# Optimization experiments

Hardware: AMD Instinct MI355X
Metric: run time of the kernel (lower is better)

## Reference

```python
import jax, jax.numpy as jnp
import numpy as np

N_NODES = 25000
N_EDGES = 400000
N_GRAPHS = 100
D_IN = 16
D = 32          # node_dim
K = 11          # spectral coefficients = edge_dim
NOUT1 = 30
NOUT2 = 2
L = 2           # n_interactions
D_OUT = 32


def setup_inputs() -> dict:
    key = jax.random.key(0)
    ks = jax.random.split(key, 24)
    s = 0.1
    inp = {
        'x': jax.random.normal(ks[0], (N_NODES, D_IN), jnp.float32),
        'edge_attr': jax.random.uniform(ks[1], (N_EDGES, K), jnp.float32),
        'edge_index': jax.random.randint(ks[2], (2, N_EDGES), 0, N_NODES),
        'batch': jnp.sort(jax.random.randint(ks[3], (N_NODES,), 0, N_GRAPHS)),
        # embedding
        'emb_w': jax.random.normal(ks[4], (D_IN, D)) * s,
        'emb_b': jnp.zeros((D,)),
        # per-interaction params, stacked on leading L axis
        'init_w': jax.random.normal(ks[5], (L, D, D)) * s,             # initial_dense (no bias)
        'e1_w': jax.random.normal(ks[6], (L, K, 2 * K)) * s,
        'e2_w': jax.random.normal(ks[7], (L, K, 2 * K)) * s,
        'e3_w': jax.random.normal(ks[8], (L, K, 2 * K)) * s,
        'e4_w': jax.random.normal(ks[9], (L, 4 * K, K)) * s,
        'conv_w': jax.random.normal(ks[10], (L, K, D, NOUT1)) * s,     # SpectConv weight (selfconn=False)
        'conv_b': jnp.zeros((L, NOUT1)),
        'att_v': jax.random.normal(ks[11], (L, D, 1)) * s,
        'skip1_w': jax.random.normal(ks[12], (L, D, NOUT2)) * s,
        'skip1_b': jnp.full((L, NOUT2), 0.01),
        'skip2_w': jax.random.normal(ks[13], (L, D, NOUT2)) * s,
        'skip2_b': jnp.full((L, NOUT2), 0.01),
        'out_w': jax.random.normal(ks[14], (L, NOUT1 + NOUT2, D)) * s,
        'out_b': jnp.full((L, D), 0.01),
        # encoder output head
        'final_w': jax.random.normal(ks[15], (D, D_OUT)) * s,
        'final_b': jnp.zeros((D_OUT,)),
    }
    return inp


def _segment_softmax(raw, dst, n):
    m = jax.ops.segment_max(raw, dst, num_segments=n)
    m = jnp.where(jnp.isfinite(m), m, 0.0)
    e = jnp.exp(raw - m[dst])
    denom = jax.ops.segment_sum(e, dst, num_segments=n)
    return e / (denom[dst] + 1e-16)


def _interaction(h, src, dst, edge_attr, p):
    (init_w, e1_w, e2_w, e3_w, e4_w, conv_w, conv_b, att_v,
     s1_w, s1_b, s2_w, s2_b, out_w, out_b) = p
    n = h.shape[0]
    h_proj = h @ init_w                                     # [N, D]
    # learned edge transform
    lin = jax.nn.relu(edge_attr @ e1_w)                     # [E, 2K]
    gate = jnp.tanh(edge_attr @ e2_w) * jnp.tanh(edge_attr @ e3_w)
    ea = jax.nn.relu(jnp.concatenate([lin, gate], axis=1) @ e4_w)  # [E, K]
    # spectral conv with attention (selfconn=False)
    xs = h_proj[src]                                        # gather [E, D]
    msgs = ea[:, :, None] * xs[:, None, :]                  # [E, K, D]
    agg = jax.ops.segment_sum(msgs, dst, num_segments=n)    # [N, K, D]
    sum_out = jnp.einsum('nkd,kdo->no', agg, conv_w)        # [N, NOUT1]
    pooled = ea.mean(axis=1, keepdims=True) * xs            # mean_k msg_k, [E, D]
    raw_att = (pooled @ att_v)[:, 0]                        # [E]
    att = _segment_softmax(raw_att, dst, n)                 # [E]
    att_agg = jax.ops.segment_sum(att[:, None, None] * msgs, dst, num_segments=n)
    att_out = jnp.einsum('nkd,kdo->no', att_agg, conv_w)
    conv_out = jax.nn.relu(sum_out + att_out + conv_b)      # [N, NOUT1]
    skip = jnp.tanh(h_proj @ s1_w + s1_b) * jnp.tanh(h_proj @ s2_w + s2_b)  # [N, NOUT2]
    layer_out = jnp.concatenate([conv_out, skip], axis=1)
    delta = layer_out @ out_w + out_b                       # [N, D]
    return delta, att


def reference(x, edge_attr, emb_w, emb_b, init_w, e1_w, e2_w, e3_w, e4_w,
              conv_w, conv_b, att_v, skip1_w, skip1_b, skip2_w, skip2_b,
              out_w, out_b, final_w, final_b, edge_index, batch):
    src, dst = edge_index[0], edge_index[1]
    h = x @ emb_w + emb_b                                   # node embedding [N, D]
    atts = []
    for l in range(L):
        p = (init_w[l], e1_w[l], e2_w[l], e3_w[l], e4_w[l], conv_w[l], conv_b[l],
             att_v[l], skip1_w[l], skip1_b[l], skip2_w[l], skip2_b[l], out_w[l], out_b[l])
        delta, att = _interaction(h, src, dst, edge_attr, p)
        h = h + delta                                       # residual
        atts.append(att)
    # global mean pool per graph
    counts = jax.ops.segment_sum(jnp.ones((h.shape[0],), h.dtype), batch, num_segments=N_GRAPHS)
    pooled = jax.ops.segment_sum(h, batch, num_segments=N_GRAPHS) / jnp.maximum(counts, 1.0)[:, None]
    output = pooled @ final_w + final_b                     # [G, D_OUT]
    return output, h, jnp.stack(atts)
```

## Files before the change

### kernel.cpp

```cpp
#include <hip/hip_runtime.h>
#include <hip/hip_bf16.h>

typedef __hip_bfloat16 bf16;
using f32x4v = __attribute__((ext_vector_type(4))) float;
using bf16x8 = __attribute__((ext_vector_type(8))) short;

#define N_NODES 25000
#define N_PAD   25024
#define N_EDGES 400000
#define N_GR    100
#define SCAN_C  25

__device__ __forceinline__ bf16 tob(float v) { return __float2bfloat16(v); }
__device__ __forceinline__ unsigned short tobu(float v) {
  union { bf16 b; unsigned short u; } c; c.b = __float2bfloat16(v); return c.u;
}
__device__ __forceinline__ float b2f(unsigned short u) { return __uint_as_float(((unsigned)u) << 16); }
__device__ __forceinline__ float tanh_fast(float x) {
  float e = __expf(2.f * x);
  return 1.f - 2.f * __builtin_amdgcn_rcpf(e + 1.f);
}

__global__ __launch_bounds__(256) void hist_kernel(const int* __restrict__ dst, int* __restrict__ deg, int E) {
  int e = blockIdx.x * blockDim.x + threadIdx.x;
  if (e < E) atomicAdd(&deg[dst[e]], 1);
}

__global__ __launch_bounds__(1024) void scan_kernel(const int* __restrict__ deg, int* __restrict__ offs,
                                                    int* __restrict__ cur, int n) {
  __shared__ int wsum[16];
  __shared__ int wpre[16];
  int t = threadIdx.x, lane = t & 63, w = t >> 6;
  int base = t * SCAN_C;
  int loc[SCAN_C];
  int s = 0;
  #pragma unroll
  for (int i = 0; i < SCAN_C; i++) {
    int idx = base + i;
    int v = (idx < n) ? deg[idx] : 0;
    loc[i] = s; s += v;
  }
  int x = s;
  #pragma unroll
  for (int sh = 1; sh < 64; sh <<= 1) { int y = __shfl_up(x, sh); if (lane >= sh) x += y; }
  if (lane == 63) wsum[w] = x;
  __syncthreads();
  if (w == 0 && lane < 16) {
    int ws_ = wsum[lane], xs = ws_;
    #pragma unroll
    for (int sh = 1; sh < 16; sh <<= 1) { int y = __shfl_up(xs, sh); if (lane >= sh) xs += y; }
    wpre[lane] = xs - ws_;
  }
  __syncthreads();
  int excl = wpre[w] + x - s;
  #pragma unroll
  for (int i = 0; i < SCAN_C; i++) {
    int idx = base + i;
    if (idx < n) { int o = excl + loc[i]; offs[idx] = o; cur[idx] = o; }
  }
  if (t == 1023) offs[n] = excl + s;
}

__global__ __launch_bounds__(256) void prep_kernel(const float* __restrict__ e1, const float* __restrict__ e2,
                                                   const float* __restrict__ e3, const float* __restrict__ e4,
                                                   const float* __restrict__ attv, const float* __restrict__ convw,
                                                   const float* __restrict__ outw,
                                                   const int* __restrict__ batch,
                                                   float* __restrict__ wE, bf16* __restrict__ Wt,
                                                   bf16* __restrict__ owB, int* __restrict__ gb,
                                                   int* __restrict__ deg) {
  int i = blockIdx.x * blockDim.x + threadIdx.x;
  if (i < N_NODES) deg[i] = 0;
  if (i < 2 * 1352) {
    int l = i / 1352, r = i % 1352;
    float v = 0.f;
    if (r < 264)       { int q = r;        int j = q / 12, k = q % 12; if (k < 11) v = e1[l*242 + k*22 + j]; }
    else if (r < 528)  { int q = r - 264;  int j = q / 12, k = q % 12; if (k < 11) v = e2[l*242 + k*22 + j]; }
    else if (r < 792)  { int q = r - 528;  int j = q / 12, k = q % 12; if (k < 11) v = e3[l*242 + k*22 + j]; }
    else if (r < 1056) { int q = r - 792;  int j = q / 12, k = q % 12; if (k < 11) v = e4[l*484 + j*11 + k]; }
    else if (r < 1320) { int q = r - 1056; int j = q / 12, k = q % 12; if (k < 11) v = e4[l*484 + (22 + j)*11 + k]; }
    else               { int d = r - 1320; v = attv[l*32 + d]; }
    wE[i] = v;
  }
  int t = i - 2 * 1352;
  if (t >= 0 && t < 2 * 32 * 352) {
    int l = t / (32 * 352), q = t % (32 * 352);
    int o = q / 352, dk = q % 352;
    int d = dk / 11, kk = dk % 11;
    float v = 0.f;
    if (o < 30) v = convw[l*10560 + (kk*32 + d)*30 + o];
    Wt[t] = tob(v);
  }
  int u = i - 2 * 1352 - 2 * 32 * 352;
  if (u >= 0 && u < 2048) {
    int l = u >> 10, rem = u & 1023;
    int hf = rem >> 9, rem2 = rem & 511;
    int lane = rem2 >> 3, j = rem2 & 7;
    int k = (lane >> 4) * 8 + j, n = lane & 15;
    owB[u] = tob(outw[l*1024 + k*32 + hf*16 + n]);
  }
  int g = i - 2 * 1352 - 2 * 32 * 352 - 2048;
  if (g >= 0 && g <= N_GR) {
    if (g == N_GR) { gb[g] = N_NODES; }
    else {
      int lo = 0, hi = N_NODES;
      while (lo < hi) { int mid = (lo + hi) >> 1; if (batch[mid] < g) lo = mid + 1; else hi = mid; }
      gb[g] = lo;
    }
  }
}

__global__ __launch_bounds__(256) void emb_hproj_kernel(const float* __restrict__ x, const float* __restrict__ w,
                                                        const float* __restrict__ b, const float* __restrict__ w1,
                                                        float* __restrict__ h, float* __restrict__ hp,
                                                        unsigned short* __restrict__ hpb, int N) {
  __shared__ float semb[16 * 32];
  __shared__ float sw1[32 * 32];
  __shared__ float sb[32];
  __shared__ float sx[8][16];
  __shared__ float sh[8][33];
  int tid = threadIdx.x;
  for (int i = tid; i < 16 * 32; i += 256) semb[i] = w[i];
  for (int i = tid; i < 32 * 32; i += 256) sw1[i] = w1[i];
  if (tid < 32) sb[tid] = b[tid];
  int nb = blockIdx.x * 8;
  if (tid < 128) {
    int n = nb + (tid >> 4), k = tid & 15;
    sx[tid >> 4][k] = (n < N) ? x[(size_t)n * 16 + k] : 0.f;
  }
  __syncthreads();
  int grp = tid >> 5, d = tid & 31;
  int n = nb + grp;
  float acc = sb[d];
  #pragma unroll
  for (int k = 0; k < 16; k++) acc += sx[grp][k] * semb[k*32 + d];
  sh[grp][d] = acc;
  if (n < N) h[(size_t)n * 32 + d] = acc;
  __syncthreads();
  float hpv = 0.f;
  #pragma unroll
  for (int k = 0; k < 32; k++) hpv += sh[grp][k] * sw1[k*32 + d];
  if (n < N) {
    hp[(size_t)n * 32 + d] = hpv;
    hpb[(size_t)n * 32 + d] = tobu(hpv);
  }
}

__device__ __forceinline__ void loadw12(const float4* base, int idx3, float* w) {
  float4 a = base[idx3], b = base[idx3 + 1], c = base[idx3 + 2];
  w[0]=a.x; w[1]=a.y; w[2]=a.z; w[3]=a.w;
  w[4]=b.x; w[5]=b.y; w[6]=b.z; w[7]=b.w;
  w[8]=c.x; w[9]=c.y; w[10]=c.z; w[11]=c.w;
}

__global__ __launch_bounds__(256) void edge_kernel(const float* __restrict__ eattr,
                                                   const int* __restrict__ srcA,
                                                   const int* __restrict__ dstA,
                                                   int* __restrict__ cur,
                                                   int* __restrict__ elist,
                                                   int* __restrict__ epos,
                                                   const unsigned short* __restrict__ hpb,
                                                   const float* __restrict__ wEl,
                                                   uint4* __restrict__ pay, int first, int E) {
  const float4* w4 = (const float4*)wEl;
  int e = blockIdx.x * blockDim.x + threadIdx.x;
  bool live = e < E;
  float a[11], acc[11];
  #pragma unroll
  for (int k = 0; k < 11; k++) {
    a[k] = live ? eattr[(size_t)e*11 + k] : 0.f;
    acc[k] = 0.f;
  }
  int pp = 0;
  if (live) {
    if (first) {
      pp = atomicAdd(&cur[dstA[e]], 1);
      elist[pp] = e;
      epos[e] = pp;
    } else {
      pp = epos[e];
    }
  }
  for (int j = 0; j < 22; j++) {
    float w[12];
    loadw12(w4, j*3, w);
    float l1 = 0.f;
    #pragma unroll
    for (int k = 0; k < 11; k++) l1 += a[k] * w[k];
    loadw12(w4, 66 + j*3, w);
    float l2 = 0.f;
    #pragma unroll
    for (int k = 0; k < 11; k++) l2 += a[k] * w[k];
    loadw12(w4, 132 + j*3, w);
    float l3 = 0.f;
    #pragma unroll
    for (int k = 0; k < 11; k++) l3 += a[k] * w[k];
    float gg = tanh_fast(l2) * tanh_fast(l3);
    l1 = fmaxf(l1, 0.f);
    float wl[12], wg[12];
    loadw12(w4, 198 + j*3, wl);
    loadw12(w4, 264 + j*3, wg);
    #pragma unroll
    for (int k = 0; k < 11; k++) acc[k] += l1*wl[k] + gg*wg[k];
  }
  if (!live) return;
  const float* av = wEl + 1320;
  float mean = 0.f;
  #pragma unroll
  for (int k = 0; k < 11; k++) { acc[k] = fmaxf(acc[k], 0.f); mean += acc[k]; }
  mean *= (1.f / 11.f);
  int s = srcA[e];
  const uint2* hb = (const uint2*)(hpb + (size_t)s * 32);
  float dot = 0.f;
  #pragma unroll
  for (int q = 0; q < 8; q++) {
    uint2 hv = hb[q];
    dot += b2f((unsigned short)hv.x) * av[q*4+0] + b2f((unsigned short)(hv.x >> 16)) * av[q*4+1]
         + b2f((unsigned short)hv.y) * av[q*4+2] + b2f((unsigned short)(hv.y >> 16)) * av[q*4+3];
  }
  float raw = mean * dot;
  unsigned p[6];
  #pragma unroll
  for (int q = 0; q < 5; q++)
    p[q] = (unsigned)tobu(acc[2*q]) | ((unsigned)tobu(acc[2*q+1]) << 16);
  p[5] = (unsigned)tobu(acc[10]);
  pay[(size_t)pp * 2]     = make_uint4(p[0], p[1], p[2], p[3]);
  pay[(size_t)pp * 2 + 1] = make_uint4(p[4], p[5], __float_as_uint(raw), (unsigned)s);
}

__device__ __forceinline__ void unpack_pay(uint4 p0, uint4 p1, float* ev) {
  ev[0] = b2f((unsigned short)p0.x); ev[1] = b2f((unsigned short)(p0.x >> 16));
  ev[2] = b2f((unsigned short)p0.y); ev[3] = b2f((unsigned short)(p0.y >> 16));
  ev[4] = b2f((unsigned short)p0.z); ev[5] = b2f((unsigned short)(p0.z >> 16));
  ev[6] = b2f((unsigned short)p0.w); ev[7] = b2f((unsigned short)(p0.w >> 16));
  ev[8] = b2f((unsigned short)p1.x); ev[9] = b2f((unsigned short)(p1.x >> 16));
  ev[10] = b2f((unsigned short)p1.y);
}

__global__ __launch_bounds__(256) void node_kernel(const int* __restrict__ offs, const int* __restrict__ elist,
                                                   const uint4* __restrict__ pay,
                                                   const unsigned short* __restrict__ hpb,
                                                   bf16* __restrict__ Abuf, float* __restrict__ atts, int N) {
  int wid = threadIdx.x >> 6, lane = threadIdx.x & 63;
  int half = lane >> 5, d = lane & 31;
  int n = blockIdx.x * 4 + wid;
  if (n >= N_PAD) return;
  int beg = 0, deg = 0;
  if (n < N) { beg = offs[n]; deg = offs[n + 1] - beg; }
  const float* payf = (const float*)pay;

  float M, inv;
  float einv_reg = 0.f;
  bool fast = (deg <= 64);
  if (fast) {
    float r = (lane < deg) ? payf[(size_t)(beg + lane) * 8 + 6] : -1e30f;
    float mm = r;
    #pragma unroll
    for (int sh = 1; sh < 64; sh <<= 1) mm = fmaxf(mm, __shfl_xor(mm, sh));
    M = mm;
    float ex = (lane < deg) ? __expf(r - M) : 0.f;
    float ss = ex;
    #pragma unroll
    for (int sh = 1; sh < 64; sh <<= 1) ss += __shfl_xor(ss, sh);
    inv = 1.f / (ss + 1e-16f);
    einv_reg = ex * inv;
    if (lane < deg) atts[elist[beg + lane]] = einv_reg;
  } else {
    float m_l = -1e30f;
    for (int jj = lane; jj < deg; jj += 64)
      m_l = fmaxf(m_l, payf[(size_t)(beg + jj) * 8 + 6]);
    #pragma unroll
    for (int sh = 1; sh < 64; sh <<= 1) m_l = fmaxf(m_l, __shfl_xor(m_l, sh));
    M = m_l;
    float s_l = 0.f;
    for (int jj = lane; jj < deg; jj += 64)
      s_l += __expf(payf[(size_t)(beg + jj) * 8 + 6] - M);
    #pragma unroll
    for (int sh = 1; sh < 64; sh <<= 1) s_l += __shfl_xor(s_l, sh);
    inv = 1.f / (s_l + 1e-16f);
    for (int jj = lane; jj < deg; jj += 64) {
      float r = payf[(size_t)(beg + jj) * 8 + 6];
      atts[elist[beg + jj]] = __expf(r - M) * inv;
    }
  }

  float agg[11];
  #pragma unroll
  for (int k = 0; k < 11; k++) agg[k] = 0.f;

  int j = half;
  for (; j + 2 < deg; j += 4) {
    uint4 a0 = pay[(size_t)(beg + j) * 2],     a1 = pay[(size_t)(beg + j) * 2 + 1];
    uint4 b0 = pay[(size_t)(beg + j + 2) * 2], b1 = pay[(size_t)(beg + j + 2) * 2 + 1];
    float xa = b2f(hpb[(size_t)(int)a1.w * 32 + d]);
    float xb = b2f(hpb[(size_t)(int)b1.w * 32 + d]);
    float ca = fast ? (1.f + __shfl(einv_reg, j))
                    : (1.f + __expf(__uint_as_float(a1.z) - M) * inv);
    float cb = fast ? (1.f + __shfl(einv_reg, j + 2))
                    : (1.f + __expf(__uint_as_float(b1.z) - M) * inv);
    float cxa = ca * xa, cxb = cb * xb;
    float eva[11], evb[11];
    unpack_pay(a0, a1, eva);
    unpack_pay(b0, b1, evb);
    #pragma unroll
    for (int k = 0; k < 11; k++) agg[k] += eva[k] * cxa + evb[k] * cxb;
  }
  for (; j < deg; j += 2) {
    uint4 q0 = pay[(size_t)(beg + j) * 2], q1 = pay[(size_t)(beg + j) * 2 + 1];
    float xs = b2f(hpb[(size_t)(int)q1.w * 32 + d]);
    float c = fast ? (1.f + __shfl(einv_reg, j))
                   : (1.f + __expf(__uint_as_float(q1.z) - M) * inv);
    float cx = c * xs;
    float ev[11];
    unpack_pay(q0, q1, ev);
    #pragma unroll
    for (int k = 0; k < 11; k++) agg[k] += ev[k] * cx;
  }

  #pragma unroll
  for (int k = 0; k < 11; k++) agg[k] += __shfl_xor(agg[k], 32);

  if (half == 0) {
    bf16* arow = Abuf + (size_t)n * 352 + d * 11;
    #pragma unroll
    for (int k = 0; k < 11; k++) arow[k] = tob(agg[k]);
  }
}

__global__ __launch_bounds__(128) void convfused_kernel(const short* __restrict__ A, const short* __restrict__ Wt,
                                                        const short* __restrict__ owB,
                                                        const float* __restrict__ hp, float* __restrict__ h,
                                                        const float* __restrict__ convb,
                                                        const float* __restrict__ s1w, const float* __restrict__ s1b,
                                                        const float* __restrict__ s2w, const float* __restrict__ s2b,
                                                        const float* __restrict__ outb,
                                                        const float* __restrict__ initw_next,
                                                        float* __restrict__ hp_out, unsigned short* __restrict__ hpb_out,
                                                        int N) {
  __shared__ short slo[32][40];
  __shared__ float sdelta[32][36];
  __shared__ float sskipw[128];
  __shared__ float sskipb[4];
  __shared__ float scb[32];
  __shared__ float sob[32];
  __shared__ float sw1[1024];
  int tid = threadIdx.x;
  if (tid < 64) sskipw[tid] = s1w[tid];
  if (tid >= 64 && tid < 128) sskipw[tid] = s2w[tid - 64];
  if (tid < 32) sob[tid] = outb[tid];
  if (tid >= 32 && tid < 64) scb[tid - 32] = (tid - 32 < 30) ? convb[tid - 32] : 0.f;
  if (tid >= 96 && tid < 100) sskipb[tid - 96] = (tid < 98) ? s1b[tid - 96] : s2b[tid - 98];
  if (initw_next) {
    for (int i = tid; i < 1024; i += 128) sw1[i] = initw_next[i];
  }
  __syncthreads();

  int wave = tid >> 6, lane = tid & 63;
  int r16 = lane & 15, kq = lane >> 4;
  int mbase = blockIdx.x * 32 + wave * 16;

  const short* arow = A + (size_t)(mbase + r16) * 352 + kq * 8;
  const short* b0p = Wt + (size_t)r16 * 352 + kq * 8;
  const short* b1p = b0p + 16 * 352;
  f32x4v acc0 = {0.f, 0.f, 0.f, 0.f}, acc1 = {0.f, 0.f, 0.f, 0.f};
  #pragma unroll
  for (int ks = 0; ks < 11; ks++) {
    bf16x8 af = *(const bf16x8*)(arow + ks * 32);
    bf16x8 b0 = *(const bf16x8*)(b0p + ks * 32);
    bf16x8 b1 = *(const bf16x8*)(b1p + ks * 32);
    acc0 = __builtin_amdgcn_mfma_f32_16x16x32_bf16(af, b0, acc0, 0, 0, 0);
    acc1 = __builtin_amdgcn_mfma_f32_16x16x32_bf16(af, b1, acc1, 0, 0, 0);
  }
  #pragma unroll
  for (int r = 0; r < 4; r++) {
    int row = wave * 16 + kq * 4 + r;
    slo[row][r16] = (short)tobu(fmaxf(acc0[r] + scb[r16], 0.f));
    if (r16 < 14) slo[row][16 + r16] = (short)tobu(fmaxf(acc1[r] + scb[16 + r16], 0.f));
  }
  __syncthreads();

  if (tid < 64) {
    int row = tid >> 1, jx = tid & 1;
    int grow = blockIdx.x * 32 + row;
    float a1 = sskipb[jx], a2 = sskipb[2 + jx];
    if (grow < N) {
      const float* hr = hp + (size_t)grow * 32;
      #pragma unroll
      for (int dd = 0; dd < 32; dd++) {
        float hv = hr[dd];
        a1 += hv * sskipw[dd*2 + jx];
        a2 += hv * sskipw[64 + dd*2 + jx];
      }
    }
    slo[row][30 + jx] = (short)tobu(tanh_fast(a1) * tanh_fast(a2));
  }
  __syncthreads();

  bf16x8 a2f = *(const bf16x8*)&slo[wave * 16 + r16][kq * 8];
  bf16x8 bo0 = *(const bf16x8*)(owB + lane * 8);
  bf16x8 bo1 = *(const bf16x8*)(owB + 512 + lane * 8);
  f32x4v d0 = {0.f, 0.f, 0.f, 0.f}, d1 = {0.f, 0.f, 0.f, 0.f};
  d0 = __builtin_amdgcn_mfma_f32_16x16x32_bf16(a2f, bo0, d0, 0, 0, 0);
  d1 = __builtin_amdgcn_mfma_f32_16x16x32_bf16(a2f, bo1, d1, 0, 0, 0);
  #pragma unroll
  for (int r = 0; r < 4; r++) {
    int row = wave * 16 + kq * 4 + r;
    sdelta[row][r16] = d0[r] + sob[r16];
    sdelta[row][16 + r16] = d1[r] + sob[16 + r16];
  }
  __syncthreads();

  int row = tid >> 2, col0 = (tid & 3) * 8;
  int grow = blockIdx.x * 32 + row;
  if (grow < N) {
    float* hr = h + (size_t)grow * 32 + col0;
    float4 ha = *(float4*)hr;
    float4 hb = *(float4*)(hr + 4);
    float4 da = *(float4*)&sdelta[row][col0];
    float4 db = *(float4*)&sdelta[row][col0 + 4];
    ha.x += da.x; ha.y += da.y; ha.z += da.z; ha.w += da.w;
    hb.x += db.x; hb.y += db.y; hb.z += db.z; hb.w += db.w;
    *(float4*)hr = ha;
    *(float4*)(hr + 4) = hb;
    *(float4*)&sdelta[row][col0] = ha;
    *(float4*)&sdelta[row][col0 + 4] = hb;
  }
  if (initw_next) {
    __syncthreads();
    if (grow < N) {
      float o[8];
      #pragma unroll
      for (int c = 0; c < 8; c++) o[c] = 0.f;
      #pragma unroll
      for (int k = 0; k < 32; k++) {
        float hv = sdelta[row][k];
        #pragma unroll
        for (int c = 0; c < 8; c++) o[c] += hv * sw1[k*32 + col0 + c];
      }
      float* hpo = hp_out + (size_t)grow * 32 + col0;
      unsigned short* hbo = hpb_out + (size_t)grow * 32 + col0;
      #pragma unroll
      for (int c = 0; c < 8; c++) { hpo[c] = o[c]; hbo[c] = tobu(o[c]); }
    }
  }
}

__global__ __launch_bounds__(256) void pool2_kernel(const float* __restrict__ h, const int* __restrict__ gb,
                                                    const float* __restrict__ fw, const float* __restrict__ fb,
                                                    float* __restrict__ out0, float* __restrict__ outh) {
  __shared__ float part[8][32];
  __shared__ float pooled[32];
  int g = blockIdx.x;
  int s = gb[g], e = gb[g + 1];
  int grp = threadIdx.x >> 5, d = threadIdx.x & 31;
  float acc = 0.f;
  for (int n = s + grp; n < e; n += 8) {
    float v = h[(size_t)n * 32 + d];
    outh[(size_t)n * 32 + d] = v;
    acc += v;
  }
  part[grp][d] = acc;
  __syncthreads();
  if (threadIdx.x < 32) {
    float sum = 0.f;
    #pragma unroll
    for (int i = 0; i < 8; i++) sum += part[i][d];
    pooled[d] = sum / fmaxf((float)(e - s), 1.f);
  }
  __syncthreads();
  if (threadIdx.x < 32) {
    int jx = threadIdx.x;
    float o = fb[jx];
    #pragma unroll
    for (int dd = 0; dd < 32; dd++) o += pooled[dd] * fw[dd*32 + jx];
    out0[g * 32 + jx] = o;
  }
}

extern "C" void kernel_launch(void* const* d_in, const int* in_sizes, int n_in,
                              void* d_out, int out_size, void* d_ws, size_t ws_size,
                              hipStream_t stream) {
  (void)in_sizes; (void)n_in; (void)out_size; (void)ws_size;
  const float* x      = (const float*)d_in[0];
  const float* eattr  = (const float*)d_in[1];
  const int* eidx     = (const int*)d_in[2];
  const int* batch    = (const int*)d_in[3];
  const float* emb_w  = (const float*)d_in[4];
  const float* emb_b  = (const float*)d_in[5];
  const float* init_w = (const float*)d_in[6];
  const float* e1w    = (const float*)d_in[7];
  const float* e2w    = (const float*)d_in[8];
  const float* e3w    = (const float*)d_in[9];
  const float* e4w    = (const float*)d_in[10];
  const float* convw  = (const float*)d_in[11];
  const float* convb  = (const float*)d_in[12];
  const float* attv   = (const float*)d_in[13];
  const float* s1w    = (const float*)d_in[14];
  const float* s1b    = (const float*)d_in[15];
  const float* s2w    = (const float*)d_in[16];
  const float* s2b    = (const float*)d_in[17];
  const float* outw   = (const float*)d_in[18];
  const float* outb   = (const float*)d_in[19];
  const float* finw   = (const float*)d_in[20];
  const float* finb   = (const float*)d_in[21];

  char* ws = (char*)d_ws;
  size_t off = 0;
  auto take = [&](size_t bytes) -> char* {
    char* p = ws + off;
    off += (bytes + 255) & ~(size_t)255;
    return p;
  };
  float* h    = (float*)take((size_t)N_NODES * 32 * 4);
  float* hp   = (float*)take((size_t)N_NODES * 32 * 4);
  unsigned short* hpb = (unsigned short*)take((size_t)N_NODES * 32 * 2);
  uint4* pay  = (uint4*)take((size_t)N_EDGES * 32);
  bf16*  Abuf = (bf16*)take((size_t)N_PAD * 352 * 2);
  int*   deg  = (int*)take((size_t)N_NODES * 4);
  int*   offs = (int*)take((size_t)(N_NODES + 1) * 4);
  int*   cur  = (int*)take((size_t)N_NODES * 4);
  int*   elist= (int*)take((size_t)N_EDGES * 4);
  int*   epos = (int*)take((size_t)N_EDGES * 4);
  int*   gb   = (int*)take((size_t)(N_GR + 1) * 4);
  float* wE   = (float*)take((size_t)2 * 1352 * 4);
  bf16*  Wt   = (bf16*)take((size_t)2 * 32 * 352 * 2);
  bf16*  owB  = (bf16*)take((size_t)2048 * 2);

  float* out0 = (float*)d_out;
  float* outh = out0 + N_GR * 32;
  float* outa = outh + (size_t)N_NODES * 32;

  const int* srcA = eidx;
  const int* dstA = eidx + N_EDGES;

  prep_kernel<<<107, 256, 0, stream>>>(e1w, e2w, e3w, e4w, attv, convw, outw, batch, wE, Wt, owB, gb, deg);
  hist_kernel<<<(N_EDGES + 255) / 256, 256, 0, stream>>>(dstA, deg, N_EDGES);
  scan_kernel<<<1, 1024, 0, stream>>>(deg, offs, cur, N_NODES);
  emb_hproj_kernel<<<(N_NODES + 7) / 8, 256, 0, stream>>>(x, emb_w, emb_b, init_w, h, hp, hpb, N_NODES);

  for (int l = 0; l < 2; l++) {
    edge_kernel<<<(N_EDGES + 255) / 256, 256, 0, stream>>>(
        eattr, srcA, dstA, cur, elist, epos, hpb, wE + l * 1352, pay, (l == 0) ? 1 : 0, N_EDGES);
    node_kernel<<<N_PAD / 4, 256, 0, stream>>>(offs, elist, pay, hpb,
                                               Abuf, outa + (size_t)l * N_EDGES, N_NODES);
    convfused_kernel<<<N_PAD / 32, 128, 0, stream>>>(
        (const short*)Abuf, (const short*)Wt + (size_t)l * 32 * 352, (const short*)owB + (size_t)l * 1024,
        hp, h, convb + l * 30, s1w + l * 64, s1b + l * 2, s2w + l * 64, s2b + l * 2,
        outb + l * 32,
        (l == 0) ? (init_w + 1024) : nullptr, hp, hpb, N_NODES);
  }

  pool2_kernel<<<N_GR, 256, 0, stream>>>(h, gb, finw, finb, out0, outh);
}
```

Baseline: 231.0 us.

## Move edge MLP to bf16 MFMA with pre-converted edge attributes

Replaces the per-thread scalar edge MLP (three 11x22 layers plus a 44x11 layer) with MFMA 16x16x32 bf16 tiles, 16 edges per wave, staging intermediates through shared memory. The histogram kernel now also converts edge attributes to padded bf16 once, through a coalesced shared-memory load, so both interaction layers read compact aligned rows. The cost being targeted is the scalar FMA work and the uniform weight loads in the edge kernel. In exchange it adds bf16 rounding of the inputs and hidden activations, extra LDS traffic, and one more kernel-side buffer.

After: 253.6 us. 9.8% more time.

```diff
diff --git a/kernel.cpp b/kernel.cpp
--- a/kernel.cpp
+++ b/kernel.cpp
@@ -21,9 +21,30 @@
   return 1.f - 2.f * __builtin_amdgcn_rcpf(e + 1.f);
 }
 
-__global__ __launch_bounds__(256) void hist_kernel(const int* __restrict__ dst, int* __restrict__ deg, int E) {
-  int e = blockIdx.x * blockDim.x + threadIdx.x;
-  if (e < E) atomicAdd(&deg[dst[e]], 1);
+__global__ __launch_bounds__(256) void hist_kernel(const float* __restrict__ eattr,
+                                                   const int* __restrict__ dst,
+                                                   int* __restrict__ deg,
+                                                   unsigned short* __restrict__ eattrB, int E) {
+  __shared__ float sx[2816];
+  long long base = (long long)blockIdx.x * 2816;
+  for (int i = threadIdx.x; i < 2816; i += 256) {
+    long long gi = base + i;
+    sx[i] = (gi < (long long)E * 11) ? eattr[gi] : 0.f;
+  }
+  __syncthreads();
+  int e = blockIdx.x * 256 + threadIdx.x;
+  if (e >= E) return;
+  atomicAdd(&deg[dst[e]], 1);
+  const float* a = &sx[threadIdx.x * 11];
+  unsigned q0 = (unsigned)tobu(a[0]) | ((unsigned)tobu(a[1]) << 16);
+  unsigned q1 = (unsigned)tobu(a[2]) | ((unsigned)tobu(a[3]) << 16);
+  unsigned q2 = (unsigned)tobu(a[4]) | ((unsigned)tobu(a[5]) << 16);
+  unsigned q3 = (unsigned)tobu(a[6]) | ((unsigned)tobu(a[7]) << 16);
+  unsigned q4 = (unsigned)tobu(a[8]) | ((unsigned)tobu(a[9]) << 16);
+  unsigned q5 = (unsigned)tobu(a[10]);
+  uint4* eb = (uint4*)(eattrB + (size_t)e * 16);
+  eb[0] = make_uint4(q0, q1, q2, q3);
+  eb[1] = make_uint4(q4, q5, 0u, 0u);
 }
 
 __global__ __launch_bounds__(1024) void scan_kernel(const int* __restrict__ deg, int* __restrict__ offs,
@@ -63,35 +84,42 @@
 
 __global__ __launch_bounds__(256) void prep_kernel(const float* __restrict__ e1, const float* __restrict__ e2,
                                                    const float* __restrict__ e3, const float* __restrict__ e4,
-                                                   const float* __restrict__ attv, const float* __restrict__ convw,
-                                                   const float* __restrict__ outw,
+                                                   const float* __restrict__ convw, const float* __restrict__ outw,
                                                    const int* __restrict__ batch,
-                                                   float* __restrict__ wE, bf16* __restrict__ Wt,
-                                                   bf16* __restrict__ owB, int* __restrict__ gb,
-                                                   int* __restrict__ deg) {
+                                                   unsigned short* __restrict__ W1B,
+                                                   unsigned short* __restrict__ W2B,
+                                                   bf16* __restrict__ Wt, bf16* __restrict__ owB,
+                                                   int* __restrict__ gb, int* __restrict__ deg) {
   int i = blockIdx.x * blockDim.x + threadIdx.x;
   if (i < N_NODES) deg[i] = 0;
-  if (i < 2 * 1352) {
-    int l = i / 1352, r = i % 1352;
+  if (i < 5120) {
+    int l = i / 2560, r = i % 2560;
+    int t = r >> 9, rem = r & 511, n16 = rem >> 5, k = rem & 31;
+    int np = t * 16 + n16;
     float v = 0.f;
-    if (r < 264)       { int q = r;        int j = q / 12, k = q % 12; if (k < 11) v = e1[l*242 + k*22 + j]; }
-    else if (r < 528)  { int q = r - 264;  int j = q / 12, k = q % 12; if (k < 11) v = e2[l*242 + k*22 + j]; }
-    else if (r < 792)  { int q = r - 528;  int j = q / 12, k = q % 12; if (k < 11) v = e3[l*242 + k*22 + j]; }
-    else if (r < 1056) { int q = r - 792;  int j = q / 12, k = q % 12; if (k < 11) v = e4[l*484 + j*11 + k]; }
-    else if (r < 1320) { int q = r - 1056; int j = q / 12, k = q % 12; if (k < 11) v = e4[l*484 + (22 + j)*11 + k]; }
-    else               { int d = r - 1320; v = attv[l*32 + d]; }
-    wE[i] = v;
-  }
-  int t = i - 2 * 1352;
-  if (t >= 0 && t < 2 * 32 * 352) {
-    int l = t / (32 * 352), q = t % (32 * 352);
+    if (k < 11 && np < 66) {
+      if (np < 22)      v = e1[l*242 + k*22 + np];
+      else if (np < 44) v = e2[l*242 + k*22 + (np - 22)];
+      else              v = e3[l*242 + k*22 + (np - 44)];
+    }
+    W1B[i] = tobu(v);
+  }
+  int j2 = i - 5120;
+  if (j2 >= 0 && j2 < 1536) {
+    int l = j2 / 768, r = j2 % 768, n = r / 48, k = r % 48;
+    float v = (n < 11 && k < 44) ? e4[l*484 + k*11 + n] : 0.f;
+    W2B[j2] = tobu(v);
+  }
+  int t_ = i - 6656;
+  if (t_ >= 0 && t_ < 22528) {
+    int l = t_ / 11264, q = t_ % 11264;
     int o = q / 352, dk = q % 352;
     int d = dk / 11, kk = dk % 11;
     float v = 0.f;
     if (o < 30) v = convw[l*10560 + (kk*32 + d)*30 + o];
-    Wt[t] = tob(v);
-  }
-  int u = i - 2 * 1352 - 2 * 32 * 352;
+    Wt[t_] = tob(v);
+  }
+  int u = i - 29184;
   if (u >= 0 && u < 2048) {
     int l = u >> 10, rem = u & 1023;
     int hf = rem >> 9, rem2 = rem & 511;
@@ -99,7 +127,7 @@
     int k = (lane >> 4) * 8 + j, n = lane & 15;
     owB[u] = tob(outw[l*1024 + k*32 + hf*16 + n]);
   }
-  int g = i - 2 * 1352 - 2 * 32 * 352 - 2048;
+  int g = i - 31232;
   if (g >= 0 && g <= N_GR) {
     if (g == N_GR) { gb[g] = N_NODES; }
     else {
@@ -146,86 +174,116 @@
   }
 }
 
-__device__ __forceinline__ void loadw12(const float4* base, int idx3, float* w) {
-  float4 a = base[idx3], b = base[idx3 + 1], c = base[idx3 + 2];
-  w[0]=a.x; w[1]=a.y; w[2]=a.z; w[3]=a.w;
-  w[4]=b.x; w[5]=b.y; w[6]=b.z; w[7]=b.w;
-  w[8]=c.x; w[9]=c.y; w[10]=c.z; w[11]=c.w;
-}
-
-__global__ __launch_bounds__(256) void edge_kernel(const float* __restrict__ eattr,
-                                                   const int* __restrict__ srcA,
-                                                   const int* __restrict__ dstA,
-                                                   int* __restrict__ cur,
-                                                   int* __restrict__ elist,
-                                                   int* __restrict__ epos,
-                                                   const unsigned short* __restrict__ hpb,
-                                                   const float* __restrict__ wEl,
-                                                   uint4* __restrict__ pay, int first, int E) {
-  const float4* w4 = (const float4*)wEl;
-  int e = blockIdx.x * blockDim.x + threadIdx.x;
-  bool live = e < E;
-  float a[11], acc[11];
-  #pragma unroll
-  for (int k = 0; k < 11; k++) {
-    a[k] = live ? eattr[(size_t)e*11 + k] : 0.f;
-    acc[k] = 0.f;
-  }
-  int pp = 0;
-  if (live) {
+__global__ __launch_bounds__(256) void edge_mfma_kernel(const unsigned short* __restrict__ eattrB,
+                                                        const unsigned short* __restrict__ W1Bl,
+                                                        const unsigned short* __restrict__ W2Bl,
+                                                        const float* __restrict__ attvl,
+                                                        const int* __restrict__ srcA,
+                                                        const int* __restrict__ dstA,
+                                                        int* __restrict__ cur,
+                                                        int* __restrict__ elist,
+                                                        int* __restrict__ epos,
+                                                        const unsigned short* __restrict__ hpb,
+                                                        uint4* __restrict__ pay, int first) {
+  __shared__ __align__(16) unsigned short sW1[5][16][40];
+  __shared__ __align__(16) unsigned short sW2[16][56];
+  __shared__ float sattv[32];
+  __shared__ float raw1[4][16][68];
+  __shared__ __align__(16) unsigned short sv[4][16][56];
+  __shared__ float sea[4][16][12];
+  int tid = threadIdx.x;
+  for (int i = tid; i < 2560; i += 256) {
+    int t = i >> 9, rem = i & 511;
+    sW1[t][rem >> 5][rem & 31] = W1Bl[i];
+  }
+  for (int i = tid; i < 768; i += 256) sW2[i / 48][i % 48] = W2Bl[i];
+  if (tid < 128) sW2[tid >> 3][48 + (tid & 7)] = 0;
+  if (tid < 32) sattv[tid] = attvl[tid];
+  __syncthreads();
+
+  int w = tid >> 6, lane = tid & 63;
+  int r16 = lane & 15, kq = lane >> 4;
+  int ebase = blockIdx.x * 64 + w * 16;
+
+  bf16x8 zz = {0, 0, 0, 0, 0, 0, 0, 0};
+  bf16x8 a1 = (kq < 2) ? *(const bf16x8*)(eattrB + (size_t)(ebase + r16) * 16 + kq * 8) : zz;
+  f32x4v c[5];
+  #pragma unroll
+  for (int t = 0; t < 5; t++) {
+    bf16x8 b = *(const bf16x8*)&sW1[t][r16][kq * 8];
+    f32x4v z4 = {0.f, 0.f, 0.f, 0.f};
+    c[t] = __builtin_amdgcn_mfma_f32_16x16x32_bf16(a1, b, z4, 0, 0, 0);
+  }
+  #pragma unroll
+  for (int t = 0; t < 5; t++) {
+    #pragma unroll
+    for (int r = 0; r < 4; r++) {
+      int col = t * 16 + r16;
+      if (col < 66) raw1[w][kq * 4 + r][col] = c[t][r];
+    }
+  }
+  {
+    int e = lane & 15, q = lane >> 4;
+    #pragma unroll
+    for (int m = 0; m < 11; m++) {
+      int i = q * 11 + m;
+      float v;
+      if (i < 22) v = fmaxf(raw1[w][e][i], 0.f);
+      else        v = tanh_fast(raw1[w][e][i]) * tanh_fast(raw1[w][e][i + 22]);
+      sv[w][e][i] = tobu(v);
+    }
+    if (q == 3) { sv[w][e][44] = 0; sv[w][e][45] = 0; sv[w][e][46] = 0; sv[w][e][47] = 0; }
+  }
+  bf16x8 a2lo = *(const bf16x8*)&sv[w][r16][kq * 8];
+  bf16x8 a2hi = (kq < 2) ? *(const bf16x8*)&sv[w][r16][32 + kq * 8] : zz;
+  bf16x8 b2lo = *(const bf16x8*)&sW2[r16][kq * 8];
+  bf16x8 b2hi = (kq < 2) ? *(const bf16x8*)&sW2[r16][32 + kq * 8] : zz;
+  f32x4v z4 = {0.f, 0.f, 0.f, 0.f};
+  f32x4v c2 = __builtin_amdgcn_mfma_f32_16x16x32_bf16(a2lo, b2lo, z4, 0, 0, 0);
+  c2 = __builtin_amdgcn_mfma_f32_16x16x32_bf16(a2hi, b2hi, c2, 0, 0, 0);
+  if (r16 < 11) {
+    #pragma unroll
+    for (int r = 0; r < 4; r++) sea[w][kq * 4 + r][r16] = fmaxf(c2[r], 0.f);
+  }
+  {
+    int e = lane >> 2, part = lane & 3;
+    int eid = ebase + e;
+    int pp = 0;
     if (first) {
-      pp = atomicAdd(&cur[dstA[e]], 1);
-      elist[pp] = e;
-      epos[e] = pp;
+      if (part == 0) { pp = atomicAdd(&cur[dstA[eid]], 1); elist[pp] = eid; epos[eid] = pp; }
+      pp = __shfl(pp, lane & ~3);
     } else {
-      pp = epos[e];
-    }
-  }
-  for (int j = 0; j < 22; j++) {
-    float w[12];
-    loadw12(w4, j*3, w);
-    float l1 = 0.f;
-    #pragma unroll
-    for (int k = 0; k < 11; k++) l1 += a[k] * w[k];
-    loadw12(w4, 66 + j*3, w);
-    float l2 = 0.f;
-    #pragma unroll
-    for (int k = 0; k < 11; k++) l2 += a[k] * w[k];
-    loadw12(w4, 132 + j*3, w);
-    float l3 = 0.f;
-    #pragma unroll
-    for (int k = 0; k < 11; k++) l3 += a[k] * w[k];
-    float gg = tanh_fast(l2) * tanh_fast(l3);
-    l1 = fmaxf(l1, 0.f);
-    float wl[12], wg[12];
-    loadw12(w4, 198 + j*3, wl);
-    loadw12(w4, 264 + j*3, wg);
-    #pragma unroll
-    for (int k = 0; k < 11; k++) acc[k] += l1*wl[k] + gg*wg[k];
-  }
-  if (!live) return;
-  const float* av = wEl + 1320;
-  float mean = 0.f;
-  #pragma unroll
-  for (int k = 0; k < 11; k++) { acc[k] = fmaxf(acc[k], 0.f); mean += acc[k]; }
-  mean *= (1.f / 11.f);
-  int s = srcA[e];
-  const uint2* hb = (const uint2*)(hpb + (size_t)s * 32);
-  float dot = 0.f;
-  #pragma unroll
-  for (int q = 0; q < 8; q++) {
-    uint2 hv = hb[q];
-    dot += b2f((unsigned short)hv.x) * av[q*4+0] + b2f((unsigned short)(hv.x >> 16)) * av[q*4+1]
-         + b2f((unsigned short)hv.y) * av[q*4+2] + b2f((unsigned short)(hv.y >> 16)) * av[q*4+3];
-  }
-  float raw = mean * dot;
-  unsigned p[6];
-  #pragma unroll
-  for (int q = 0; q < 5; q++)
-    p[q] = (unsigned)tobu(acc[2*q]) | ((unsigned)tobu(acc[2*q+1]) << 16);
-  p[5] = (unsigned)tobu(acc[10]);
-  pay[(size_t)pp * 2]     = make_uint4(p[0], p[1], p[2], p[3]);
-  pay[(size_t)pp * 2 + 1] = make_uint4(p[4], p[5], __float_as_uint(raw), (unsigned)s);
+      pp = epos[eid];
+    }
+    float msum = 0.f;
+    #pragma unroll
+    for (int m = 0; m < 3; m++) { int idx = part * 3 + m; if (idx < 11) msum += sea[w][e][idx]; }
+    msum += __shfl_xor(msum, 1);
+    msum += __shfl_xor(msum, 2);
+    float mean = msum * (1.f / 11.f);
+    int s = srcA[eid];
+    const uint2* hb = (const uint2*)(hpb + (size_t)s * 32 + part * 8);
+    uint2 h0 = hb[0], h1 = hb[1];
+    const float* av = sattv + part * 8;
+    float dot = b2f((unsigned short)h0.x) * av[0] + b2f((unsigned short)(h0.x >> 16)) * av[1]
+              + b2f((unsigned short)h0.y) * av[2] + b2f((unsigned short)(h0.y >> 16)) * av[3]
+              + b2f((unsigned short)h1.x) * av[4] + b2f((unsigned short)(h1.x >> 16)) * av[5]
+              + b2f((unsigned short)h1.y) * av[6] + b2f((unsigned short)(h1.y >> 16)) * av[7];
+    dot += __shfl_xor(dot, 1);
+    dot += __shfl_xor(dot, 2);
+    float raw = mean * dot;
+    if (part == 0) {
+      unsigned q0 = (unsigned)tobu(sea[w][e][0]) | ((unsigned)tobu(sea[w][e][1]) << 16);
+      unsigned q1 = (unsigned)tobu(sea[w][e][2]) | ((unsigned)tobu(sea[w][e][3]) << 16);
+      unsigned q2 = (unsigned)tobu(sea[w][e][4]) | ((unsigned)tobu(sea[w][e][5]) << 16);
+      unsigned q3 = (unsigned)tobu(sea[w][e][6]) | ((unsigned)tobu(sea[w][e][7]) << 16);
+      pay[(size_t)pp * 2] = make_uint4(q0, q1, q2, q3);
+    } else if (part == 1) {
+      unsigned q4 = (unsigned)tobu(sea[w][e][8]) | ((unsigned)tobu(sea[w][e][9]) << 16);
+      unsigned q5 = (unsigned)tobu(sea[w][e][10]);
+      pay[(size_t)pp * 2 + 1] = make_uint4(q4, q5, __float_as_uint(raw), (unsigned)s);
+    }
+  }
 }
 
 __device__ __forceinline__ void unpack_pay(uint4 p0, uint4 p1, float* ev) {
@@ -515,6 +573,7 @@
   float* hp   = (float*)take((size_t)N_NODES * 32 * 4);
   unsigned short* hpb = (unsigned short*)take((size_t)N_NODES * 32 * 2);
   uint4* pay  = (uint4*)take((size_t)N_EDGES * 32);
+  unsigned short* eattrB = (unsigned short*)take((size_t)N_EDGES * 16 * 2);
   bf16*  Abuf = (bf16*)take((size_t)N_PAD * 352 * 2);
   int*   deg  = (int*)take((size_t)N_NODES * 4);
   int*   offs = (int*)take((size_t)(N_NODES + 1) * 4);
@@ -522,7 +581,8 @@
   int*   elist= (int*)take((size_t)N_EDGES * 4);
   int*   epos = (int*)take((size_t)N_EDGES * 4);
   int*   gb   = (int*)take((size_t)(N_GR + 1) * 4);
-  float* wE   = (float*)take((size_t)2 * 1352 * 4);
+  unsigned short* W1B = (unsigned short*)take((size_t)2 * 2560 * 2);
+  unsigned short* W2B = (unsigned short*)take((size_t)2 * 768 * 2);
   bf16*  Wt   = (bf16*)take((size_t)2 * 32 * 352 * 2);
   bf16*  owB  = (bf16*)take((size_t)2048 * 2);
 
@@ -533,14 +593,16 @@
   const int* srcA = eidx;
   const int* dstA = eidx + N_EDGES;
 
-  prep_kernel<<<107, 256, 0, stream>>>(e1w, e2w, e3w, e4w, attv, convw, outw, batch, wE, Wt, owB, gb, deg);
-  hist_kernel<<<(N_EDGES + 255) / 256, 256, 0, stream>>>(dstA, deg, N_EDGES);
+  prep_kernel<<<123, 256, 0, stream>>>(e1w, e2w, e3w, e4w, convw, outw, batch,
+                                       W1B, W2B, Wt, owB, gb, deg);
+  hist_kernel<<<(N_EDGES + 255) / 256, 256, 0, stream>>>(eattr, dstA, deg, eattrB, N_EDGES);
   scan_kernel<<<1, 1024, 0, stream>>>(deg, offs, cur, N_NODES);
   emb_hproj_kernel<<<(N_NODES + 7) / 8, 256, 0, stream>>>(x, emb_w, emb_b, init_w, h, hp, hpb, N_NODES);
 
   for (int l = 0; l < 2; l++) {
-    edge_kernel<<<(N_EDGES + 255) / 256, 256, 0, stream>>>(
-        eattr, srcA, dstA, cur, elist, epos, hpb, wE + l * 1352, pay, (l == 0) ? 1 : 0, N_EDGES);
+    edge_mfma_kernel<<<N_EDGES / 64, 256, 0, stream>>>(
+        eattrB, W1B + (size_t)l * 2560, W2B + (size_t)l * 768, attv + l * 32,
+        srcA, dstA, cur, elist, epos, hpb, pay, (l == 0) ? 1 : 0);
     node_kernel<<<N_PAD / 4, 256, 0, stream>>>(offs, elist, pay, hpb,
                                                Abuf, outa + (size_t)l * N_EDGES, N_NODES);
     convfused_kernel<<<N_PAD / 32, 128, 0, stream>>>(
```

## Pre-permute edge attributes into destination-sorted bf16 buffer in a dedicated fill kernel

Applied to the files above, without the earlier changes.

A new fill_kernel does the CSR atomic scatter once. It stages edge_attr through shared memory for coalesced loads, converts it to bf16, and writes it together with the source index into a compact 32-byte record at the sorted position. The edge kernel then reads these records contiguously in sorted order and writes its payload contiguously too. This replaces the strided fp32 reads and the scattered payload writes, and drops the epos indirection in both layers. The cost is an extra kernel launch and a 12.8 MB buffer. Rounding edge attributes to bf16 before the edge MLP also adds precision error.

Result: slower. 254.9 us (+10.4%).

```diff
diff --git a/kernel.cpp b/kernel.cpp
--- a/kernel.cpp
+++ b/kernel.cpp
@@ -59,6 +59,34 @@
     if (idx < n) { int o = excl + loc[i]; offs[idx] = o; cur[idx] = o; }
   }
   if (t == 1023) offs[n] = excl + s;
+}
+
+__global__ __launch_bounds__(256) void fill_kernel(const float* __restrict__ eattr,
+                                                   const int* __restrict__ srcA,
+                                                   const int* __restrict__ dstA,
+                                                   int* __restrict__ cur,
+                                                   int* __restrict__ elist,
+                                                   uint4* __restrict__ eattrC, int E) {
+  __shared__ float sx[2816];
+  long long base = (long long)blockIdx.x * 2816;
+  for (int i = threadIdx.x; i < 2816; i += 256) {
+    long long gi = base + i;
+    sx[i] = (gi < (long long)E * 11) ? eattr[gi] : 0.f;
+  }
+  __syncthreads();
+  int e = blockIdx.x * 256 + threadIdx.x;
+  if (e >= E) return;
+  int p = atomicAdd(&cur[dstA[e]], 1);
+  elist[p] = e;
+  const float* a = &sx[threadIdx.x * 11];
+  unsigned q0 = (unsigned)tobu(a[0]) | ((unsigned)tobu(a[1]) << 16);
+  unsigned q1 = (unsigned)tobu(a[2]) | ((unsigned)tobu(a[3]) << 16);
+  unsigned q2 = (unsigned)tobu(a[4]) | ((unsigned)tobu(a[5]) << 16);
+  unsigned q3 = (unsigned)tobu(a[6]) | ((unsigned)tobu(a[7]) << 16);
+  unsigned q4 = (unsigned)tobu(a[8]) | ((unsigned)tobu(a[9]) << 16);
+  unsigned q5 = (unsigned)tobu(a[10]);
+  eattrC[(size_t)p * 2]     = make_uint4(q0, q1, q2, q3);
+  eattrC[(size_t)p * 2 + 1] = make_uint4(q4, q5, (unsigned)srcA[e], 0u);
 }
 
 __global__ __launch_bounds__(256) void prep_kernel(const float* __restrict__ e1, const float* __restrict__ e2,
@@ -153,34 +181,26 @@
   w[8]=c.x; w[9]=c.y; w[10]=c.z; w[11]=c.w;
 }
 
-__global__ __launch_bounds__(256) void edge_kernel(const float* __restrict__ eattr,
-                                                   const int* __restrict__ srcA,
-                                                   const int* __restrict__ dstA,
-                                                   int* __restrict__ cur,
-                                                   int* __restrict__ elist,
-                                                   int* __restrict__ epos,
+__global__ __launch_bounds__(256) void edge_kernel(const uint4* __restrict__ eattrC,
                                                    const unsigned short* __restrict__ hpb,
                                                    const float* __restrict__ wEl,
-                                                   uint4* __restrict__ pay, int first, int E) {
+                                                   uint4* __restrict__ pay, int E) {
   const float4* w4 = (const float4*)wEl;
-  int e = blockIdx.x * blockDim.x + threadIdx.x;
-  bool live = e < E;
-  float a[11], acc[11];
-  #pragma unroll
-  for (int k = 0; k < 11; k++) {
-    a[k] = live ? eattr[(size_t)e*11 + k] : 0.f;
-    acc[k] = 0.f;
-  }
-  int pp = 0;
-  if (live) {
-    if (first) {
-      pp = atomicAdd(&cur[dstA[e]], 1);
-      elist[pp] = e;
-      epos[e] = pp;
-    } else {
-      pp = epos[e];
-    }
-  }
+  int p = blockIdx.x * blockDim.x + threadIdx.x;
+  if (p >= E) return;
+  uint4 c0 = eattrC[(size_t)p * 2];
+  uint4 c1 = eattrC[(size_t)p * 2 + 1];
+  float a[11];
+  a[0] = b2f((unsigned short)c0.x); a[1] = b2f((unsigned short)(c0.x >> 16));
+  a[2] = b2f((unsigned short)c0.y); a[3] = b2f((unsigned short)(c0.y >> 16));
+  a[4] = b2f((unsigned short)c0.z); a[5] = b2f((unsigned short)(c0.z >> 16));
+  a[6] = b2f((unsigned short)c0.w); a[7] = b2f((unsigned short)(c0.w >> 16));
+  a[8] = b2f((unsigned short)c1.x); a[9] = b2f((unsigned short)(c1.x >> 16));
+  a[10] = b2f((unsigned short)c1.y);
+  int s = (int)c1.z;
+  float acc[11];
+  #pragma unroll
+  for (int k = 0; k < 11; k++) acc[k] = 0.f;
   for (int j = 0; j < 22; j++) {
     float w[12];
     loadw12(w4, j*3, w);
@@ -203,13 +223,11 @@
     #pragma unroll
     for (int k = 0; k < 11; k++) acc[k] += l1*wl[k] + gg*wg[k];
   }
-  if (!live) return;
   const float* av = wEl + 1320;
   float mean = 0.f;
   #pragma unroll
   for (int k = 0; k < 11; k++) { acc[k] = fmaxf(acc[k], 0.f); mean += acc[k]; }
   mean *= (1.f / 11.f);
-  int s = srcA[e];
   const uint2* hb = (const uint2*)(hpb + (size_t)s * 32);
   float dot = 0.f;
   #pragma unroll
@@ -219,13 +237,13 @@
          + b2f((unsigned short)hv.y) * av[q*4+2] + b2f((unsigned short)(hv.y >> 16)) * av[q*4+3];
   }
   float raw = mean * dot;
-  unsigned p[6];
-  #pragma unroll
-  for (int q = 0; q < 5; q++)
-    p[q] = (unsigned)tobu(acc[2*q]) | ((unsigned)tobu(acc[2*q+1]) << 16);
-  p[5] = (unsigned)tobu(acc[10]);
-  pay[(size_t)pp * 2]     = make_uint4(p[0], p[1], p[2], p[3]);
-  pay[(size_t)pp * 2 + 1] = make_uint4(p[4], p[5], __float_as_uint(raw), (unsigned)s);
+  unsigned q[6];
+  #pragma unroll
+  for (int m = 0; m < 5; m++)
+    q[m] = (unsigned)tobu(acc[2*m]) | ((unsigned)tobu(acc[2*m+1]) << 16);
+  q[5] = (unsigned)tobu(acc[10]);
+  pay[(size_t)p * 2]     = make_uint4(q[0], q[1], q[2], q[3]);
+  pay[(size_t)p * 2 + 1] = make_uint4(q[4], q[5], __float_as_uint(raw), (unsigned)s);
 }
 
 __device__ __forceinline__ void unpack_pay(uint4 p0, uint4 p1, float* ev) {
@@ -515,12 +533,12 @@
   float* hp   = (float*)take((size_t)N_NODES * 32 * 4);
   unsigned short* hpb = (unsigned short*)take((size_t)N_NODES * 32 * 2);
   uint4* pay  = (uint4*)take((size_t)N_EDGES * 32);
+  uint4* eattrC = (uint4*)take((size_t)N_EDGES * 32);
   bf16*  Abuf = (bf16*)take((size_t)N_PAD * 352 * 2);
   int*   deg  = (int*)take((size_t)N_NODES * 4);
   int*   offs = (int*)take((size_t)(N_NODES + 1) * 4);
   int*   cur  = (int*)take((size_t)N_NODES * 4);
   int*   elist= (int*)take((size_t)N_EDGES * 4);
-  int*   epos = (int*)take((size_t)N_EDGES * 4);
   int*   gb   = (int*)take((size_t)(N_GR + 1) * 4);
   float* wE   = (float*)take((size_t)2 * 1352 * 4);
   bf16*  Wt   = (bf16*)take((size_t)2 * 32 * 352 * 2);
@@ -536,11 +554,12 @@
   prep_kernel<<<107, 256, 0, stream>>>(e1w, e2w, e3w, e4w, attv, convw, outw, batch, wE, Wt, owB, gb, deg);
   hist_kernel<<<(N_EDGES + 255) / 256, 256, 0, stream>>>(dstA, deg, N_EDGES);
   scan_kernel<<<1, 1024, 0, stream>>>(deg, offs, cur, N_NODES);
+  fill_kernel<<<(N_EDGES + 255) / 256, 256, 0, stream>>>(eattr, srcA, dstA, cur, elist, eattrC, N_EDGES);
   emb_hproj_kernel<<<(N_NODES + 7) / 8, 256, 0, stream>>>(x, emb_w, emb_b, init_w, h, hp, hpb, N_NODES);
 
   for (int l = 0; l < 2; l++) {
     edge_kernel<<<(N_EDGES + 255) / 256, 256, 0, stream>>>(
-        eattr, srcA, dstA, cur, elist, epos, hpb, wE + l * 1352, pay, (l == 0) ? 1 : 0, N_EDGES);
+        eattrC, hpb, wE + l * 1352, pay, N_EDGES);
     node_kernel<<<N_PAD / 4, 256, 0, stream>>>(offs, elist, pay, hpb,
                                                Abuf, outa + (size_t)l * N_EDGES, N_NODES);
     convfused_kernel<<<N_PAD / 32, 128, 0, stream>>>(
```

## Compute both layers' edge MLPs in one pass and split out attention raw

Applied to the files above, without the earlier changes.

The edge MLP depends only on edge attributes, so both interaction layers' edge features are now computed in a single kernel that reads edge_attr once and writes two CSR-ordered payload buffers. The attention logit, which needs the updated node projection, moves into a light per-layer kernel that reads mean and src from the payload and patches in the raw score. This removes one full read of edge attributes and the epos indirection, at the cost of a second payload buffer, higher register pressure from two accumulator sets, and an extra kernel launch per layer.

Result: slower. 241.5 us (+4.6%).

```diff
diff --git a/kernel.cpp b/kernel.cpp
--- a/kernel.cpp
+++ b/kernel.cpp
@@ -153,79 +153,99 @@
   w[8]=c.x; w[9]=c.y; w[10]=c.z; w[11]=c.w;
 }
 
-__global__ __launch_bounds__(256) void edge_kernel(const float* __restrict__ eattr,
-                                                   const int* __restrict__ srcA,
-                                                   const int* __restrict__ dstA,
-                                                   int* __restrict__ cur,
-                                                   int* __restrict__ elist,
-                                                   int* __restrict__ epos,
-                                                   const unsigned short* __restrict__ hpb,
-                                                   const float* __restrict__ wEl,
-                                                   uint4* __restrict__ pay, int first, int E) {
-  const float4* w4 = (const float4*)wEl;
+__global__ __launch_bounds__(256) void edge_mlp_kernel(const float* __restrict__ eattr,
+                                                       const int* __restrict__ srcA,
+                                                       const int* __restrict__ dstA,
+                                                       int* __restrict__ cur,
+                                                       int* __restrict__ elist,
+                                                       const float* __restrict__ wE0,
+                                                       const float* __restrict__ wE1,
+                                                       uint4* __restrict__ pay0,
+                                                       uint4* __restrict__ pay1, int E) {
+  const float4* wa = (const float4*)wE0;
+  const float4* wb = (const float4*)wE1;
   int e = blockIdx.x * blockDim.x + threadIdx.x;
   bool live = e < E;
-  float a[11], acc[11];
+  float a[11], acc0[11], acc1[11];
   #pragma unroll
   for (int k = 0; k < 11; k++) {
     a[k] = live ? eattr[(size_t)e*11 + k] : 0.f;
-    acc[k] = 0.f;
-  }
-  int pp = 0;
+    acc0[k] = 0.f; acc1[k] = 0.f;
+  }
+  int pp = 0, s = 0;
   if (live) {
-    if (first) {
-      pp = atomicAdd(&cur[dstA[e]], 1);
-      elist[pp] = e;
-      epos[e] = pp;
-    } else {
-      pp = epos[e];
-    }
+    s = srcA[e];
+    pp = atomicAdd(&cur[dstA[e]], 1);
+    elist[pp] = e;
   }
   for (int j = 0; j < 22; j++) {
-    float w[12];
-    loadw12(w4, j*3, w);
-    float l1 = 0.f;
-    #pragma unroll
-    for (int k = 0; k < 11; k++) l1 += a[k] * w[k];
-    loadw12(w4, 66 + j*3, w);
-    float l2 = 0.f;
-    #pragma unroll
-    for (int k = 0; k < 11; k++) l2 += a[k] * w[k];
-    loadw12(w4, 132 + j*3, w);
-    float l3 = 0.f;
-    #pragma unroll
-    for (int k = 0; k < 11; k++) l3 += a[k] * w[k];
-    float gg = tanh_fast(l2) * tanh_fast(l3);
-    l1 = fmaxf(l1, 0.f);
-    float wl[12], wg[12];
-    loadw12(w4, 198 + j*3, wl);
-    loadw12(w4, 264 + j*3, wg);
-    #pragma unroll
-    for (int k = 0; k < 11; k++) acc[k] += l1*wl[k] + gg*wg[k];
+    float wA[12], wB[12], wC[12];
+    loadw12(wa, j*3, wA);
+    loadw12(wa, 66 + j*3, wB);
+    loadw12(wa, 132 + j*3, wC);
+    float l1a = 0.f, l2a = 0.f, l3a = 0.f;
+    #pragma unroll
+    for (int k = 0; k < 11; k++) { l1a += a[k]*wA[k]; l2a += a[k]*wB[k]; l3a += a[k]*wC[k]; }
+    loadw12(wb, j*3, wA);
+    loadw12(wb, 66 + j*3, wB);
+    loadw12(wb, 132 + j*3, wC);
+    float l1b = 0.f, l2b = 0.f, l3b = 0.f;
+    #pragma unroll
+    for (int k = 0; k < 11; k++) { l1b += a[k]*wA[k]; l2b += a[k]*wB[k]; l3b += a[k]*wC[k]; }
+    float gga = tanh_fast(l2a) * tanh_fast(l3a);
+    float ggb = tanh_fast(l2b) * tanh_fast(l3b);
+    l1a = fmaxf(l1a, 0.f);
+    l1b = fmaxf(l1b, 0.f);
+    loadw12(wa, 198 + j*3, wA);
+    loadw12(wa, 264 + j*3, wB);
+    #pragma unroll
+    for (int k = 0; k < 11; k++) acc0[k] += l1a*wA[k] + gga*wB[k];
+    loadw12(wb, 198 + j*3, wA);
+    loadw12(wb, 264 + j*3, wB);
+    #pragma unroll
+    for (int k = 0; k < 11; k++) acc1[k] += l1b*wA[k] + ggb*wB[k];
   }
   if (!live) return;
-  const float* av = wEl + 1320;
-  float mean = 0.f;
-  #pragma unroll
-  for (int k = 0; k < 11; k++) { acc[k] = fmaxf(acc[k], 0.f); mean += acc[k]; }
-  mean *= (1.f / 11.f);
-  int s = srcA[e];
+  float mean0 = 0.f, mean1 = 0.f;
+  #pragma unroll
+  for (int k = 0; k < 11; k++) {
+    acc0[k] = fmaxf(acc0[k], 0.f); mean0 += acc0[k];
+    acc1[k] = fmaxf(acc1[k], 0.f); mean1 += acc1[k];
+  }
+  mean0 *= (1.f / 11.f);
+  mean1 *= (1.f / 11.f);
+  unsigned q[6];
+  #pragma unroll
+  for (int m = 0; m < 5; m++)
+    q[m] = (unsigned)tobu(acc0[2*m]) | ((unsigned)tobu(acc0[2*m+1]) << 16);
+  q[5] = (unsigned)tobu(acc0[10]);
+  pay0[(size_t)pp * 2]     = make_uint4(q[0], q[1], q[2], q[3]);
+  pay0[(size_t)pp * 2 + 1] = make_uint4(q[4], q[5], __float_as_uint(mean0), (unsigned)s);
+  #pragma unroll
+  for (int m = 0; m < 5; m++)
+    q[m] = (unsigned)tobu(acc1[2*m]) | ((unsigned)tobu(acc1[2*m+1]) << 16);
+  q[5] = (unsigned)tobu(acc1[10]);
+  pay1[(size_t)pp * 2]     = make_uint4(q[0], q[1], q[2], q[3]);
+  pay1[(size_t)pp * 2 + 1] = make_uint4(q[4], q[5], __float_as_uint(mean1), (unsigned)s);
+}
+
+__global__ __launch_bounds__(256) void edge_raw_kernel(uint4* __restrict__ pay,
+                                                       const unsigned short* __restrict__ hpb,
+                                                       const float* __restrict__ attvl, int E) {
+  int p = blockIdx.x * blockDim.x + threadIdx.x;
+  if (p >= E) return;
+  uint4 m1 = pay[(size_t)p * 2 + 1];
+  float mean = __uint_as_float(m1.z);
+  int s = (int)m1.w;
   const uint2* hb = (const uint2*)(hpb + (size_t)s * 32);
   float dot = 0.f;
   #pragma unroll
   for (int q = 0; q < 8; q++) {
     uint2 hv = hb[q];
-    dot += b2f((unsigned short)hv.x) * av[q*4+0] + b2f((unsigned short)(hv.x >> 16)) * av[q*4+1]
-         + b2f((unsigned short)hv.y) * av[q*4+2] + b2f((unsigned short)(hv.y >> 16)) * av[q*4+3];
-  }
-  float raw = mean * dot;
-  unsigned p[6];
-  #pragma unroll
-  for (int q = 0; q < 5; q++)
-    p[q] = (unsigned)tobu(acc[2*q]) | ((unsigned)tobu(acc[2*q+1]) << 16);
-  p[5] = (unsigned)tobu(acc[10]);
-  pay[(size_t)pp * 2]     = make_uint4(p[0], p[1], p[2], p[3]);
-  pay[(size_t)pp * 2 + 1] = make_uint4(p[4], p[5], __float_as_uint(raw), (unsigned)s);
+    dot += b2f((unsigned short)hv.x) * attvl[q*4+0] + b2f((unsigned short)(hv.x >> 16)) * attvl[q*4+1]
+         + b2f((unsigned short)hv.y) * attvl[q*4+2] + b2f((unsigned short)(hv.y >> 16)) * attvl[q*4+3];
+  }
+  ((float*)pay)[(size_t)p * 8 + 6] = mean * dot;
 }
 
 __device__ __forceinline__ void unpack_pay(uint4 p0, uint4 p1, float* ev) {
@@ -514,13 +534,13 @@
   float* h    = (float*)take((size_t)N_NODES * 32 * 4);
   float* hp   = (float*)take((size_t)N_NODES * 32 * 4);
   unsigned short* hpb = (unsigned short*)take((size_t)N_NODES * 32 * 2);
-  uint4* pay  = (uint4*)take((size_t)N_EDGES * 32);
+  uint4* pay0 = (uint4*)take((size_t)N_EDGES * 32);
+  uint4* pay1 = (uint4*)take((size_t)N_EDGES * 32);
   bf16*  Abuf = (bf16*)take((size_t)N_PAD * 352 * 2);
   int*   deg  = (int*)take((size_t)N_NODES * 4);
   int*   offs = (int*)take((size_t)(N_NODES + 1) * 4);
   int*   cur  = (int*)take((size_t)N_NODES * 4);
   int*   elist= (int*)take((size_t)N_EDGES * 4);
-  int*   epos = (int*)take((size_t)N_EDGES * 4);
   int*   gb   = (int*)take((size_t)(N_GR + 1) * 4);
   float* wE   = (float*)take((size_t)2 * 1352 * 4);
   bf16*  Wt   = (bf16*)take((size_t)2 * 32 * 352 * 2);
@@ -536,11 +556,14 @@
   prep_kernel<<<107, 256, 0, stream>>>(e1w, e2w, e3w, e4w, attv, convw, outw, batch, wE, Wt, owB, gb, deg);
   hist_kernel<<<(N_EDGES + 255) / 256, 256, 0, stream>>>(dstA, deg, N_EDGES);
   scan_kernel<<<1, 1024, 0, stream>>>(deg, offs, cur, N_NODES);
+  edge_mlp_kernel<<<(N_EDGES + 255) / 256, 256, 0, stream>>>(
+      eattr, srcA, dstA, cur, elist, wE, wE + 1352, pay0, pay1, N_EDGES);
   emb_hproj_kernel<<<(N_NODES + 7) / 8, 256, 0, stream>>>(x, emb_w, emb_b, init_w, h, hp, hpb, N_NODES);
 
   for (int l = 0; l < 2; l++) {
-    edge_kernel<<<(N_EDGES + 255) / 256, 256, 0, stream>>>(
-        eattr, srcA, dstA, cur, elist, epos, hpb, wE + l * 1352, pay, (l == 0) ? 1 : 0, N_EDGES);
+    uint4* pay = (l == 0) ? pay0 : pay1;
+    edge_raw_kernel<<<(N_EDGES + 255) / 256, 256, 0, stream>>>(
+        pay, hpb, wE + l * 1352 + 1320, N_EDGES);
     node_kernel<<<N_PAD / 4, 256, 0, stream>>>(offs, elist, pay, hpb,
                                                Abuf, outa + (size_t)l * N_EDGES, N_NODES);
     convfused_kernel<<<N_PAD / 32, 128, 0, stream>>>(
```
